# Kernel optimization log

Measured on AMD Instinct MI355X. Metric: run time of the kernel, lower is better.

## Reference

```python
import jax, jax.numpy as jnp
import numpy as np

G, K = 5, 3          # spline intervals, spline order
NB = G + K           # number of B-spline basis functions per edge
WIDTH = [12, 64, 64, 24]


def make_grid(in_dim):
    # pykan default grid on [-1,1], extended by K knots on each side
    h = 2.0 / G
    base = np.linspace(-1.0, 1.0, G + 1)
    left = base[0] - h * np.arange(K, 0, -1)
    right = base[-1] + h * np.arange(1, K + 1)
    g = np.concatenate([left, base, right]).astype(np.float32)  # (G+2K+1,)
    return jnp.asarray(np.tile(g[None, :], (in_dim, 1)))          # (in, G+2K+1)


def b_spline_basis(x, grid):
    """Cox-de Boor recursion. x: (N, in); grid: (in, G+2K+1) -> (N, in, G+K)."""
    xe = x[..., None]                     # (N, in, 1)
    g = grid[None]                        # (1, in, G+2K+1)
    B = ((xe >= g[..., :-1]) & (xe < g[..., 1:])).astype(x.dtype)  # degree 0
    for d in range(1, K + 1):
        B = ((xe - g[..., : -(d + 1)]) / (g[..., d:-1] - g[..., : -(d + 1)])) * B[..., :-1] \
          + ((g[..., d + 1:] - xe) / (g[..., d + 1:] - g[..., 1:-d])) * B[..., 1:]
    return B                              # (N, in, G+K)


def kan_layer(x, grid, coef, scale_base, scale_sp):
    # x: (N, in); coef: (in, out, G+K); scale_base/scale_sp: (in, out)
    B = b_spline_basis(x, grid)                               # (N, in, G+K)
    # fold scale_sp into coef to avoid materializing (N, in, out)
    y_spline = jnp.einsum('nig,iog->no', B, coef * scale_sp[:, :, None])
    y_base = jax.nn.silu(x) @ scale_base                      # (N, out)
    return y_base + y_spline


def setup_inputs() -> dict:
    key = jax.random.key(0)
    ks = jax.random.split(key, 10)
    x = jax.random.normal(ks[0], (32, 12, 64, 64), dtype=jnp.float32)
    inp = {'x': x}
    ki = 1
    for li in range(3):
        din, dout = WIDTH[li], WIDTH[li + 1]
        inp[f'grid{li}'] = make_grid(din)
        inp[f'coef{li}'] = 0.1 * jax.random.normal(ks[ki], (din, dout, NB), dtype=jnp.float32); ki += 1
        inp[f'sb{li}'] = (1.0 / np.sqrt(din)) * jnp.ones((din, dout), jnp.float32) \
                         + 0.1 * jax.random.normal(ks[ki], (din, dout), dtype=jnp.float32); ki += 1
        inp[f'ss{li}'] = jnp.ones((din, dout), jnp.float32)
    return inp


def reference(x, grid0, coef0, sb0, ss0, grid1, coef1, sb1, ss1, grid2, coef2, sb2, ss2):
    B, C, H, W = x.shape
    h = jnp.transpose(x, (0, 2, 3, 1)).reshape(-1, C)  # (B*H*W, C) per-pixel rows
    h = kan_layer(h, grid0, coef0, sb0, ss0)
    h = kan_layer(h, grid1, coef1, sb1, ss1)
    h = kan_layer(h, grid2, coef2, sb2, ss2)
    out_c = h.shape[-1]
    return jnp.transpose(h.reshape(B, H, W, out_c), (0, 3, 1, 2))
```

## Files before the change

### kernel.cpp

```cpp
#include <hip/hip_runtime.h>
#include <hip/hip_bf16.h>
#include <math.h>

#define D0 12
#define D1 64
#define D2 64
#define D3 24
#define HWP 4096
#define NROWS (32 * HWP)

#define ROWS 32
#define BLK 256

#define K0 128
#define K1 576
#define K2 576
#define S0c (K0/32)
#define S1c (K1/32)
#define S2c (K2/32)
#define T0c 4
#define T1c 4
#define T2c 2

#define WE0 (S0c*T0c*64*8)
#define WE1 (S1c*T1c*64*8)
#define WE2 (S2c*T2c*64*8)
#define WE_ALL (WE0+WE1+WE2)
#define WBYTES (2*WE_ALL*sizeof(unsigned short))

typedef __attribute__((ext_vector_type(8))) short short8;
typedef __attribute__((ext_vector_type(4))) float float4v;

__device__ __align__(16) unsigned short g_Wfb[2 * WE_ALL];

__device__ __forceinline__ unsigned short f2bf(float f) {
    unsigned int b = __float_as_uint(f);
    unsigned int r = (b + 0x7FFFu + ((b >> 16) & 1u)) >> 16;
    return (unsigned short)r;
}
__device__ __forceinline__ float bf2f(unsigned short u) {
    return __uint_as_float(((unsigned int)u) << 16);
}
__device__ __forceinline__ unsigned short f2bf_fast(float f) {
    __hip_bfloat16 h = __float2bfloat16(f);
    return reinterpret_cast<unsigned short&>(h);
}

__global__ void pack_w(unsigned short* __restrict__ Wpk,
                       const float* __restrict__ c0, const float* __restrict__ b0, const float* __restrict__ s0_,
                       const float* __restrict__ c1, const float* __restrict__ b1, const float* __restrict__ s1_,
                       const float* __restrict__ c2, const float* __restrict__ b2, const float* __restrict__ s2_) {
    int idx = blockIdx.x * 256 + threadIdx.x;
    if (idx >= WE_ALL) return;
    int base, T, in, out;
    const float *cf, *sb, *ss;
    if (idx < WE0)            { base = idx;             T = T0c; in = D0; out = D1; cf = c0; sb = b0; ss = s0_; }
    else if (idx < WE0 + WE1) { base = idx - WE0;       T = T1c; in = D1; out = D2; cf = c1; sb = b1; ss = s1_; }
    else                      { base = idx - WE0 - WE1; T = T2c; in = D2; out = D3; cf = c2; sb = b2; ss = s2_; }
    int j  = base & 7;
    int l  = (base >> 3) & 63;
    int st = base >> 9;
    int t  = st % T;
    int s  = st / T;
    int k  = 32 * s + 8 * (l >> 4) + j;
    int o  = 16 * t + (l & 15);
    float w = 0.0f;
    int i = k / 9, g = k % 9;
    if (i < in && o < out)
        w = (g < 8) ? cf[(i * out + o) * 8 + g] * ss[i * out + o] : sb[i * out + o];
    unsigned short hi = f2bf(w);
    unsigned short lo = f2bf(w - bf2f(hi));
    Wpk[idx] = hi;
    Wpk[idx + WE_ALL] = lo;
}

__device__ __forceinline__ float sgpr(float x) {
    return __uint_as_float(__builtin_amdgcn_readfirstlane(__float_as_uint(x)));
}

#define MFMA16(a, b, c) __builtin_amdgcn_mfma_f32_16x16x32_bf16((a), (b), (c), 0, 0, 0)

#define LDA(m, s) (*(const short8*)(pb + ((((16*(m) + r15) * 1152) + 64*(s) + 16*kg) ^ swA)))

template <int NS, int T>
__device__ __forceinline__ void mfma_layer(const unsigned short* __restrict__ WH,
                                           const unsigned short* __restrict__ WL,
                                           int w, int lane, int r15, int kg, int swA,
                                           const char* pb, float4v& acc0, float4v& acc1) {
    short8 wh[NS], wl[NS];
#pragma unroll
    for (int s = 0; s < (NS < 2 ? NS : 2); ++s) {
        wh[s] = *(const short8*)(WH + (((size_t)(s * T + w) * 64 + lane) * 8));
        wl[s] = *(const short8*)(WL + (((size_t)(s * T + w) * 64 + lane) * 8));
    }
#pragma unroll
    for (int s = 0; s < NS; ++s) {
        if (s + 2 < NS) {
            wh[s + 2] = *(const short8*)(WH + (((size_t)((s + 2) * T + w) * 64 + lane) * 8));
            wl[s + 2] = *(const short8*)(WL + (((size_t)((s + 2) * T + w) * 64 + lane) * 8));
        }
        short8 a0 = LDA(0, s);
        short8 a1 = LDA(1, s);
        acc0 = MFMA16(a0, wh[s], acc0);
        acc0 = MFMA16(a0, wl[s], acc0);
        acc1 = MFMA16(a1, wh[s], acc1);
        acc1 = MFMA16(a1, wl[s], acc1);
    }
}

__global__ __launch_bounds__(BLK, 4) void kan_mfma(const float* __restrict__ X,
                                                   float* __restrict__ Y,
                                                   const float* __restrict__ grid,
                                                   const unsigned short* __restrict__ Wpk) {
    __shared__ __align__(16) unsigned short panel[ROWS * 576];
    char* pb = (char*)&panel[0];

    const int tid  = threadIdx.x;
    const int lane = tid & 63;
    const int w    = tid >> 6;
    const int r15  = lane & 15;
    const int kg   = lane >> 4;
    const int swA  = (r15 & 7) << 4;

    const int b  = blockIdx.x >> 7;
    const int p0 = (blockIdx.x & 127) * 32;

    const float g0   = sgpr(grid[0]);
    const float invh = sgpr(1.0f / (grid[4] - grid[3]));

    auto writeEval = [&](int R, int i, float v) {
        float t = (v - g0) * invh;
        float cf = floorf(t);
        int c = (int)cf;
        float u = t - cf;
        bool inr = (t >= 0.0f) && (c <= 10);
        float u2 = u * u, u3 = u2 * u;
        float omu = 1.0f - u;
        float P[4];
        P[0] = omu * omu * omu * (1.0f / 6.0f);
        P[1] = (4.0f / 6.0f) + (0.5f * u3 - u2);
        P[2] = (1.0f / 6.0f) + 0.5f * (u + u2 - u3);
        P[3] = u3 * (1.0f / 6.0f);
        int sw = (R & 7) << 4;
        int rb = R * 1152 + 18 * i;
        if (inr) {
#pragma unroll
            for (int d = 0; d < 4; ++d) {
                int j = c - 3 + d;
                if ((unsigned)j < 8u)
                    *(unsigned short*)(pb + ((rb + 2 * j) ^ sw)) = f2bf_fast(P[d]);
            }
        }
        float s = v / (1.0f + __expf(-v));
        *(unsigned short*)(pb + ((rb + 16) ^ sw)) = f2bf_fast(s);
    };

    auto zeroPanel = [&] {
        float4v z = {0.f, 0.f, 0.f, 0.f};
#pragma unroll
        for (int q = 0; q < 9; ++q)
            *(float4v*)(pb + (tid * 16 + q * 4096)) = z;
    };

    const unsigned short* WH0 = Wpk;
    const unsigned short* WH1 = Wpk + WE0;
    const unsigned short* WH2 = Wpk + WE0 + WE1;
    const unsigned short* WL0 = Wpk + WE_ALL;
    const unsigned short* WL1 = Wpk + WE_ALL + WE0;
    const unsigned short* WL2 = Wpk + WE_ALL + WE0 + WE1;

    zeroPanel();
    __syncthreads();
    {
        int R = tid & 31, i = tid >> 5;
        writeEval(R, i, X[(b * D0 + i) * HWP + p0 + R]);
        if (tid < 128) {
            int R2 = (tid + 256) & 31, i2 = (tid + 256) >> 5;
            writeEval(R2, i2, X[(b * D0 + i2) * HWP + p0 + R2]);
        }
    }
    __syncthreads();

    float4v acc0 = {0.f, 0.f, 0.f, 0.f}, acc1 = {0.f, 0.f, 0.f, 0.f};
    mfma_layer<S0c, T0c>(WH0, WL0, w, lane, r15, kg, swA, pb, acc0, acc1);
    __syncthreads();

    zeroPanel();
    __syncthreads();
#pragma unroll
    for (int m = 0; m < 2; ++m)
#pragma unroll
        for (int reg = 0; reg < 4; ++reg) {
            int R = 16 * m + 4 * kg + reg;
            int c = 16 * w + r15;
            writeEval(R, c, m == 0 ? acc0[reg] : acc1[reg]);
        }
    __syncthreads();

    acc0 = (float4v){0.f, 0.f, 0.f, 0.f}; acc1 = (float4v){0.f, 0.f, 0.f, 0.f};
    mfma_layer<S1c, T1c>(WH1, WL1, w, lane, r15, kg, swA, pb, acc0, acc1);
    __syncthreads();

    zeroPanel();
    __syncthreads();
#pragma unroll
    for (int m = 0; m < 2; ++m)
#pragma unroll
        for (int reg = 0; reg < 4; ++reg) {
            int R = 16 * m + 4 * kg + reg;
            int c = 16 * w + r15;
            writeEval(R, c, m == 0 ? acc0[reg] : acc1[reg]);
        }
    __syncthreads();

    acc0 = (float4v){0.f, 0.f, 0.f, 0.f}; acc1 = (float4v){0.f, 0.f, 0.f, 0.f};
    if (w < 2)
        mfma_layer<S2c, T2c>(WH2, WL2, w, lane, r15, kg, swA, pb, acc0, acc1);
    __syncthreads();

    float* fp = (float*)pb;
    if (w < 2) {
#pragma unroll
        for (int m = 0; m < 2; ++m)
#pragma unroll
            for (int reg = 0; reg < 4; ++reg) {
                int R = 16 * m + 4 * kg + reg;
                int c = 16 * w + r15;
                if (c < D3) fp[c * 32 + R] = (m == 0 ? acc0[reg] : acc1[reg]);
            }
    }
    __syncthreads();
#pragma unroll
    for (int q = 0; q < 3; ++q) {
        int idx = tid + BLK * q;
        int c = idx >> 5, R = idx & 31;
        Y[(b * D3 + c) * HWP + p0 + R] = fp[idx];
    }
}

extern "C" void kernel_launch(void* const* d_in, const int* in_sizes, int n_in,
                              void* d_out, int out_size, void* d_ws, size_t ws_size,
                              hipStream_t stream) {
    const float* X     = (const float*)d_in[0];
    const float* grid0 = (const float*)d_in[1];
    const float* coef0 = (const float*)d_in[2];
    const float* sb0   = (const float*)d_in[3];
    const float* ss0   = (const float*)d_in[4];
    const float* coef1 = (const float*)d_in[6];
    const float* sb1   = (const float*)d_in[7];
    const float* ss1   = (const float*)d_in[8];
    const float* coef2 = (const float*)d_in[10];
    const float* sb2   = (const float*)d_in[11];
    const float* ss2   = (const float*)d_in[12];
    float* Yout = (float*)d_out;

    unsigned short* W = (unsigned short*)d_ws;
    if (ws_size < WBYTES) {
        void* sym = nullptr;
        hipGetSymbolAddress(&sym, HIP_SYMBOL(g_Wfb));
        W = (unsigned short*)sym;
    }

    hipLaunchKernelGGL(pack_w, dim3((WE_ALL + 255) / 256), dim3(256), 0, stream, W,
                       coef0, sb0, ss0, coef1, sb1, ss1, coef2, sb2, ss2);
    hipLaunchKernelGGL(kan_mfma, dim3(NROWS / ROWS), dim3(BLK), 0, stream,
                       X, Yout, grid0, W);
}
```

Measured before the change: 141.2 us.

## Repack spline panel as contiguous 8-wide blocks and drop panel zeroing

Changes the K-layout of the shared A-panel from interleaved 9-per-input (8 basis + silu) to eight contiguous basis entries per input followed by a separate silu region. Each evaluation now writes one 16-byte vector holding the four shifted nonzero basis values, which covers zeros as well, so the full-panel zeroing passes and their barriers go away. Only a small pad region is cleared once. The MFMA loop uses separate hi/lo accumulators to break the dependency chain and raises wave priority around it, and the output staging stride is padded to 33 to avoid bank conflicts.

Measured after the change: 139.8 us. No clear change (-1.0%).

```diff
diff --git a/kernel.cpp b/kernel.cpp
--- a/kernel.cpp
+++ b/kernel.cpp
@@ -30,6 +30,7 @@
 
 typedef __attribute__((ext_vector_type(8))) short short8;
 typedef __attribute__((ext_vector_type(4))) float float4v;
+typedef __attribute__((ext_vector_type(2))) unsigned long long ull2;
 
 __device__ __align__(16) unsigned short g_Wfb[2 * WE_ALL];
 
@@ -65,9 +66,15 @@
     int k  = 32 * s + 8 * (l >> 4) + j;
     int o  = 16 * t + (l & 15);
     float w = 0.0f;
-    int i = k / 9, g = k % 9;
-    if (i < in && o < out)
-        w = (g < 8) ? cf[(i * out + o) * 8 + g] * ss[i * out + o] : sb[i * out + o];
+    if (o < out) {
+        if (k < 8 * in) {
+            int i = k >> 3, g = k & 7;
+            w = cf[(i * out + o) * 8 + g] * ss[i * out + o];
+        } else if (k < 9 * in) {
+            int i = k - 8 * in;
+            w = sb[i * out + o];
+        }
+    }
     unsigned short hi = f2bf(w);
     unsigned short lo = f2bf(w - bf2f(hi));
     Wpk[idx] = hi;
@@ -86,26 +93,32 @@
 __device__ __forceinline__ void mfma_layer(const unsigned short* __restrict__ WH,
                                            const unsigned short* __restrict__ WL,
                                            int w, int lane, int r15, int kg, int swA,
-                                           const char* pb, float4v& acc0, float4v& acc1) {
+                                           const char* pb, float4v& o0, float4v& o1) {
     short8 wh[NS], wl[NS];
 #pragma unroll
     for (int s = 0; s < (NS < 2 ? NS : 2); ++s) {
         wh[s] = *(const short8*)(WH + (((size_t)(s * T + w) * 64 + lane) * 8));
         wl[s] = *(const short8*)(WL + (((size_t)(s * T + w) * 64 + lane) * 8));
     }
+    float4v a0h = {0.f,0.f,0.f,0.f}, a0l = {0.f,0.f,0.f,0.f};
+    float4v a1h = {0.f,0.f,0.f,0.f}, a1l = {0.f,0.f,0.f,0.f};
+    __builtin_amdgcn_s_setprio(1);
 #pragma unroll
     for (int s = 0; s < NS; ++s) {
         if (s + 2 < NS) {
             wh[s + 2] = *(const short8*)(WH + (((size_t)((s + 2) * T + w) * 64 + lane) * 8));
             wl[s + 2] = *(const short8*)(WL + (((size_t)((s + 2) * T + w) * 64 + lane) * 8));
         }
-        short8 a0 = LDA(0, s);
-        short8 a1 = LDA(1, s);
-        acc0 = MFMA16(a0, wh[s], acc0);
-        acc0 = MFMA16(a0, wl[s], acc0);
-        acc1 = MFMA16(a1, wh[s], acc1);
-        acc1 = MFMA16(a1, wl[s], acc1);
-    }
+        short8 A0 = LDA(0, s);
+        short8 A1 = LDA(1, s);
+        a0h = MFMA16(A0, wh[s], a0h);
+        a0l = MFMA16(A0, wl[s], a0l);
+        a1h = MFMA16(A1, wh[s], a1h);
+        a1l = MFMA16(A1, wl[s], a1l);
+    }
+    __builtin_amdgcn_s_setprio(0);
+    o0 = a0h + a0l;
+    o1 = a1h + a1l;
 }
 
 __global__ __launch_bounds__(BLK, 4) void kan_mfma(const float* __restrict__ X,
@@ -128,38 +141,34 @@
     const float g0   = sgpr(grid[0]);
     const float invh = sgpr(1.0f / (grid[4] - grid[3]));
 
-    auto writeEval = [&](int R, int i, float v) {
+    auto writeEval = [&](int R, int i, float v, int siluBase) {
         float t = (v - g0) * invh;
-        float cf = floorf(t);
-        int c = (int)cf;
-        float u = t - cf;
+        float cfl = floorf(t);
+        int c = (int)cfl;
+        float u = t - cfl;
+        float u2 = u * u, u3 = u2 * u, omu = 1.0f - u;
+        float P0f = omu * omu * omu * (1.0f / 6.0f);
+        float P1f = (4.0f / 6.0f) + (0.5f * u3 - u2);
+        float P2f = (1.0f / 6.0f) + 0.5f * (u + u2 - u3);
+        float P3f = u3 * (1.0f / 6.0f);
+        unsigned int lo32 = ((unsigned int)f2bf_fast(P1f) << 16) | f2bf_fast(P0f);
+        unsigned int hi32 = ((unsigned int)f2bf_fast(P3f) << 16) | f2bf_fast(P2f);
+        unsigned long long p64 = ((unsigned long long)hi32 << 32) | lo32;
         bool inr = (t >= 0.0f) && (c <= 10);
-        float u2 = u * u, u3 = u2 * u;
-        float omu = 1.0f - u;
-        float P[4];
-        P[0] = omu * omu * omu * (1.0f / 6.0f);
-        P[1] = (4.0f / 6.0f) + (0.5f * u3 - u2);
-        P[2] = (1.0f / 6.0f) + 0.5f * (u + u2 - u3);
-        P[3] = u3 * (1.0f / 6.0f);
+        int cc = inr ? c : 3;
+        int sh = 16 * cc - 48;
+        unsigned long long l  = p64 << (sh & 63);
+        unsigned long long rr = p64 >> ((-sh) & 63);
+        unsigned long long h  = p64 >> ((64 - sh) & 63);
+        unsigned long long h2 = p64 << ((sh - 64) & 63);
+        unsigned long long r0 = sh < 0 ? rr : (sh < 64 ? l : 0ull);
+        unsigned long long r1 = sh >= 64 ? h2 : (sh > 0 ? h : 0ull);
+        if (!inr) { r0 = 0ull; r1 = 0ull; }
         int sw = (R & 7) << 4;
-        int rb = R * 1152 + 18 * i;
-        if (inr) {
-#pragma unroll
-            for (int d = 0; d < 4; ++d) {
-                int j = c - 3 + d;
-                if ((unsigned)j < 8u)
-                    *(unsigned short*)(pb + ((rb + 2 * j) ^ sw)) = f2bf_fast(P[d]);
-            }
-        }
+        ull2 o2; o2[0] = r0; o2[1] = r1;
+        *(ull2*)(pb + ((R * 1152 + 16 * i) ^ sw)) = o2;
         float s = v / (1.0f + __expf(-v));
-        *(unsigned short*)(pb + ((rb + 16) ^ sw)) = f2bf_fast(s);
-    };
-
-    auto zeroPanel = [&] {
-        float4v z = {0.f, 0.f, 0.f, 0.f};
-#pragma unroll
-        for (int q = 0; q < 9; ++q)
-            *(float4v*)(pb + (tid * 16 + q * 4096)) = z;
+        *(unsigned short*)(pb + ((R * 1152 + siluBase + 2 * i) ^ sw)) = f2bf_fast(s);
     };
 
     const unsigned short* WH0 = Wpk;
@@ -169,47 +178,48 @@
     const unsigned short* WL1 = Wpk + WE_ALL + WE0;
     const unsigned short* WL2 = Wpk + WE_ALL + WE0 + WE1;
 
-    zeroPanel();
-    __syncthreads();
+    if (tid < 96) {
+        int r = tid / 3, part = tid % 3;
+        int sw = (r & 7) << 4;
+        char* base = pb + r * 1152;
+        if (part == 0) *(unsigned long long*)(base + (216 ^ sw)) = 0ull;
+        else if (part == 1) { ull2 z; z[0] = 0; z[1] = 0; *(ull2*)(base + (224 ^ sw)) = z; }
+        else                { ull2 z; z[0] = 0; z[1] = 0; *(ull2*)(base + (240 ^ sw)) = z; }
+    }
     {
         int R = tid & 31, i = tid >> 5;
-        writeEval(R, i, X[(b * D0 + i) * HWP + p0 + R]);
+        writeEval(R, i, X[(b * D0 + i) * HWP + p0 + R], 192);
         if (tid < 128) {
             int R2 = (tid + 256) & 31, i2 = (tid + 256) >> 5;
-            writeEval(R2, i2, X[(b * D0 + i2) * HWP + p0 + R2]);
-        }
-    }
-    __syncthreads();
-
-    float4v acc0 = {0.f, 0.f, 0.f, 0.f}, acc1 = {0.f, 0.f, 0.f, 0.f};
+            writeEval(R2, i2, X[(b * D0 + i2) * HWP + p0 + R2], 192);
+        }
+    }
+    __syncthreads();
+
+    float4v acc0, acc1;
     mfma_layer<S0c, T0c>(WH0, WL0, w, lane, r15, kg, swA, pb, acc0, acc1);
     __syncthreads();
 
-    zeroPanel();
-    __syncthreads();
 #pragma unroll
     for (int m = 0; m < 2; ++m)
 #pragma unroll
         for (int reg = 0; reg < 4; ++reg) {
             int R = 16 * m + 4 * kg + reg;
-            int c = 16 * w + r15;
-            writeEval(R, c, m == 0 ? acc0[reg] : acc1[reg]);
-        }
-    __syncthreads();
-
-    acc0 = (float4v){0.f, 0.f, 0.f, 0.f}; acc1 = (float4v){0.f, 0.f, 0.f, 0.f};
+            int ccol = 16 * w + r15;
+            writeEval(R, ccol, m == 0 ? acc0[reg] : acc1[reg], 1024);
+        }
+    __syncthreads();
+
     mfma_layer<S1c, T1c>(WH1, WL1, w, lane, r15, kg, swA, pb, acc0, acc1);
     __syncthreads();
 
-    zeroPanel();
-    __syncthreads();
 #pragma unroll
     for (int m = 0; m < 2; ++m)
 #pragma unroll
         for (int reg = 0; reg < 4; ++reg) {
             int R = 16 * m + 4 * kg + reg;
-            int c = 16 * w + r15;
-            writeEval(R, c, m == 0 ? acc0[reg] : acc1[reg]);
+            int ccol = 16 * w + r15;
+            writeEval(R, ccol, m == 0 ? acc0[reg] : acc1[reg], 1024);
         }
     __syncthreads();
 
@@ -225,16 +235,16 @@
 #pragma unroll
             for (int reg = 0; reg < 4; ++reg) {
                 int R = 16 * m + 4 * kg + reg;
-                int c = 16 * w + r15;
-                if (c < D3) fp[c * 32 + R] = (m == 0 ? acc0[reg] : acc1[reg]);
+                int ccol = 16 * w + r15;
+                if (ccol < D3) fp[ccol * 33 + R] = (m == 0 ? acc0[reg] : acc1[reg]);
             }
     }
     __syncthreads();
 #pragma unroll
     for (int q = 0; q < 3; ++q) {
         int idx = tid + BLK * q;
-        int c = idx >> 5, R = idx & 31;
-        Y[(b * D3 + c) * HWP + p0 + R] = fp[idx];
+        int ccol = idx >> 5, R = idx & 31;
+        Y[(b * D3 + ccol) * HWP + p0 + R] = fp[ccol * 33 + R];
     }
 }
 
```
